# Optimization experiments

Hardware: AMD Instinct MI355X
Metric: run time of the kernel (lower is better)

Reference implementation:

```python
import jax, jax.numpy as jnp
import numpy as np


def setup_inputs() -> dict:
    key = jax.random.key(0)
    ks = jax.random.split(key, 6)
    B, Nab, Nag, d, K = 16, 16384, 16384, 128, 10
    return {
        "H1": jax.random.normal(ks[0], (B, Nab, d), jnp.float32),
        "H2": jax.random.normal(ks[1], (B, Nag, d), jnp.float32),
        "X1": jax.random.normal(ks[2], (B, Nab, 3), jnp.float32),
        "X2": jax.random.normal(ks[3], (B, Nag, 3), jnp.float32),
        "W1": jax.random.uniform(ks[4], (K, d, d), jnp.float32),
        "W2": jax.random.uniform(ks[5], (K, d, d), jnp.float32),
    }


def _kabsch(P, Q):
    # Rigid alignment: find R (3x3), t (3,) s.t. P @ R + t ~= Q (least squares).
    c1 = P.mean(axis=0)
    c2 = Q.mean(axis=0)
    Pc = P - c1
    Qc = Q - c2
    Hm = Pc.T @ Qc  # [3,3] covariance
    U, S, Vt = jnp.linalg.svd(Hm, full_matrices=False)
    sign = jnp.sign(jnp.linalg.det(U @ Vt))
    Dm = jnp.diag(jnp.concatenate([jnp.ones(2, dtype=P.dtype), sign[None]]))
    R = U @ Dm @ Vt
    t = c2 - c1 @ R
    return P @ R + t, R, t


def reference(H1, H2, X1, X2, W1, W2):
    # Keypoint cross-attention. Faithful to torch:
    #   alpha_1k = softmax( (H1 @ W1_k @ H2.T).mean(dim=1) / sqrt(d) )
    # Using mean-over-columns identity: (H1 @ W @ H2.T).mean(1) = H1 @ W @ mean(H2,0)
    d = H1.shape[-1]
    scale = 1.0 / np.sqrt(d)
    h2bar = H2.mean(axis=1)  # [B, d]
    h1bar = H1.mean(axis=1)  # [B, d]
    v1 = jnp.einsum('kde,be->bkd', W1, h2bar)          # W1_k @ mean(H2)
    s1 = jnp.einsum('bnd,bkd->bkn', H1, v1) * scale     # [B, K, Nab]
    a1 = jax.nn.softmax(s1, axis=-1)
    Y1 = jnp.einsum('bkn,bnc->bkc', a1, X1)             # [B, K, 3]
    v2 = jnp.einsum('kde,be->bkd', W2, h1bar)
    s2 = jnp.einsum('bmd,bkd->bkm', H2, v2) * scale     # [B, K, Nag]
    a2 = jax.nn.softmax(s2, axis=-1)
    Y2 = jnp.einsum('bkm,bmc->bkc', a2, X2)             # [B, K, 3]
    Y1_aligned, R, t = jax.vmap(_kabsch)(Y1, Y2)
    return jnp.stack([Y1, Y2, Y1_aligned], axis=1)      # [B, 3, K, 3]
```

## Files before the change

### kernel.cpp

```cpp
#include <hip/hip_runtime.h>
#include <math.h>

#define NB 16
#define NN 16384
#define DD 128
#define KK 10

#define WS_FLOATS 46336

__global__ __launch_bounds__(256) void k_means(const float* __restrict__ H1,
                                               const float* __restrict__ H2,
                                               float* __restrict__ hsum) {
    int bi = blockIdx.x;
    int t = bi >> 10;
    int rem = bi & 1023;
    int b = rem >> 6;
    int chunk = rem & 63;
    const float* src = (t ? H2 : H1) + ((size_t)b * NN + (size_t)chunk * 256) * DD;
    const float4* src4 = (const float4*)src;
    int tid = threadIdx.x;
    float4 s = make_float4(0.f, 0.f, 0.f, 0.f);
#pragma unroll 8
    for (int i = 0; i < 32; ++i) {
        float4 x = src4[i * 256 + tid];
        s.x += x.x; s.y += x.y; s.z += x.z; s.w += x.w;
    }
    s.x += __shfl_xor(s.x, 32);
    s.y += __shfl_xor(s.y, 32);
    s.z += __shfl_xor(s.z, 32);
    s.w += __shfl_xor(s.w, 32);
    __shared__ float red[4][32][4];
    int wave = tid >> 6, lane = tid & 63;
    if (lane < 32) {
        red[wave][lane][0] = s.x; red[wave][lane][1] = s.y;
        red[wave][lane][2] = s.z; red[wave][lane][3] = s.w;
    }
    __syncthreads();
    if (tid < 32) {
        float t0 = 0.f, t1 = 0.f, t2 = 0.f, t3 = 0.f;
#pragma unroll
        for (int w = 0; w < 4; ++w) {
            t0 += red[w][tid][0]; t1 += red[w][tid][1];
            t2 += red[w][tid][2]; t3 += red[w][tid][3];
        }
        float* dst = hsum + (size_t)(t * NB + b) * DD + tid * 4;
        atomicAdd(dst + 0, t0);
        atomicAdd(dst + 1, t1);
        atomicAdd(dst + 2, t2);
        atomicAdd(dst + 3, t3);
    }
}

__global__ __launch_bounds__(128) void k_v(const float* __restrict__ W1,
                                           const float* __restrict__ W2,
                                           const float* __restrict__ hsum,
                                           float* __restrict__ v) {
    int bi = blockIdx.x;
    int p = bi / 160;
    int rem = bi % 160;
    int b = rem / 10;
    int k = rem % 10;
    const float* W = (p ? W2 : W1) + (size_t)k * DD * DD;
    const float* hb = hsum + (size_t)((1 - p) * NB + b) * DD;
    __shared__ float4 h_s[32];
    int tid = threadIdx.x;
    if (tid < 32) h_s[tid] = ((const float4*)hb)[tid];
    __syncthreads();
    const float4* Wrow = (const float4*)(W + (size_t)tid * DD);
    float acc = 0.f;
#pragma unroll 8
    for (int e4 = 0; e4 < 32; ++e4) {
        float4 w4 = Wrow[e4];
        float4 h4 = h_s[e4];
        acc += w4.x * h4.x + w4.y * h4.y + w4.z * h4.z + w4.w * h4.w;
    }
    const float SCALE = (float)(1.0 / (16384.0 * 11.313708498984761));
    v[((size_t)(p * NB + b) * KK + k) * DD + tid] = acc * SCALE;
}

__global__ __launch_bounds__(256) void k_scores(const float* __restrict__ H1,
                                                const float* __restrict__ H2,
                                                const float* __restrict__ X1,
                                                const float* __restrict__ X2,
                                                const float* __restrict__ v,
                                                float* __restrict__ accg) {
    int bi = blockIdx.x;
    int p = bi >> 11;
    int rem = bi & 2047;
    int b = rem >> 7;
    int tile = rem & 127;
    int row0 = tile << 7;
    const float* H = (p ? H2 : H1) + (size_t)b * NN * DD;
    const float* X = (p ? X2 : X1) + (size_t)b * NN * 3;
    const float* vp = v + (size_t)(p * NB + b) * KK * DD;

    __shared__ float4 v_s4[KK * DD / 4];
    __shared__ float red[4][40];
    float* v_s = (float*)v_s4;

    int tid = threadIdx.x;
    for (int i = tid; i < KK * DD / 4; i += 256)
        v_s4[i] = ((const float4*)vp)[i];
    __syncthreads();

    int g = tid >> 3;
    int l = tid & 7;
    int nbase = row0 + (g << 2);

    float accs[4][KK];
#pragma unroll
    for (int r = 0; r < 4; ++r)
#pragma unroll
        for (int k = 0; k < KK; ++k) accs[r][k] = 0.f;

#pragma unroll
    for (int j = 0; j < 4; ++j) {
        float4 h[4];
#pragma unroll
        for (int r = 0; r < 4; ++r)
            h[r] = *(const float4*)(H + (size_t)(nbase + r) * DD + (j << 5) + (l << 2));
#pragma unroll
        for (int k = 0; k < KK; ++k) {
            float4 vv = *(const float4*)(v_s + k * DD + (j << 5) + (l << 2));
#pragma unroll
            for (int r = 0; r < 4; ++r)
                accs[r][k] += h[r].x * vv.x + h[r].y * vv.y + h[r].z * vv.z + h[r].w * vv.w;
        }
    }
#pragma unroll
    for (int r = 0; r < 4; ++r)
#pragma unroll
        for (int k = 0; k < KK; ++k) {
            float s = accs[r][k];
            s += __shfl_xor(s, 1);
            s += __shfl_xor(s, 2);
            s += __shfl_xor(s, 4);
            accs[r][k] = s;
        }

    float pSE[KK], pY0[KK], pY1[KK], pY2[KK];
#pragma unroll
    for (int k = 0; k < KK; ++k) { pSE[k] = 0.f; pY0[k] = 0.f; pY1[k] = 0.f; pY2[k] = 0.f; }

#pragma unroll
    for (int r = 0; r < 4; ++r) {
        int n = nbase + r;
        float x0 = X[(size_t)n * 3 + 0];
        float x1 = X[(size_t)n * 3 + 1];
        float x2 = X[(size_t)n * 3 + 2];
#pragma unroll
        for (int k = 0; k < KK; ++k) {
            float e = __expf(accs[r][k]);
            pSE[k] += e;
            pY0[k] += e * x0;
            pY1[k] += e * x1;
            pY2[k] += e * x2;
        }
    }
#pragma unroll
    for (int k = 0; k < KK; ++k) {
        pSE[k] += __shfl_xor(pSE[k], 8);  pSE[k] += __shfl_xor(pSE[k], 16);  pSE[k] += __shfl_xor(pSE[k], 32);
        pY0[k] += __shfl_xor(pY0[k], 8);  pY0[k] += __shfl_xor(pY0[k], 16);  pY0[k] += __shfl_xor(pY0[k], 32);
        pY1[k] += __shfl_xor(pY1[k], 8);  pY1[k] += __shfl_xor(pY1[k], 16);  pY1[k] += __shfl_xor(pY1[k], 32);
        pY2[k] += __shfl_xor(pY2[k], 8);  pY2[k] += __shfl_xor(pY2[k], 16);  pY2[k] += __shfl_xor(pY2[k], 32);
    }
    int wave = tid >> 6, lane = tid & 63;
    if (lane == 0) {
#pragma unroll
        for (int k = 0; k < KK; ++k) {
            red[wave][k] = pSE[k];
            red[wave][10 + k] = pY0[k];
            red[wave][20 + k] = pY1[k];
            red[wave][30 + k] = pY2[k];
        }
    }
    __syncthreads();
    if (tid < 40) {
        float s = red[0][tid] + red[1][tid] + red[2][tid] + red[3][tid];
        atomicAdd(accg + (size_t)(p * NB + b) * 40 + tid, s);
    }
}

__global__ __launch_bounds__(64) void k_final(const float* __restrict__ accg,
                                              float* __restrict__ out) {
    int b = blockIdx.x;
    int tid = threadIdx.x;
    __shared__ float Ys[2][KK][3];
    if (tid < 2 * KK * 3) {
        int p = tid / 30;
        int r = tid % 30;
        int k = r / 3;
        int c = r % 3;
        const float* a = accg + (size_t)(p * NB + b) * 40;
        float val = a[10 + c * 10 + k] / a[k];
        Ys[p][k][c] = val;
        out[((size_t)(b * 3 + p) * KK + k) * 3 + c] = val;
    }
    __syncthreads();
    if (tid == 0) {
        double P[KK][3], Q[KK][3];
        double c1[3] = {0, 0, 0}, c2[3] = {0, 0, 0};
        for (int i = 0; i < KK; ++i)
            for (int c = 0; c < 3; ++c) {
                P[i][c] = (double)Ys[0][i][c];
                Q[i][c] = (double)Ys[1][i][c];
                c1[c] += P[i][c];
                c2[c] += Q[i][c];
            }
        for (int c = 0; c < 3; ++c) { c1[c] /= KK; c2[c] /= KK; }
        double A0[3][3];
        for (int a = 0; a < 3; ++a)
            for (int c = 0; c < 3; ++c) {
                double s = 0;
                for (int i = 0; i < KK; ++i) s += (P[i][a] - c1[a]) * (Q[i][c] - c2[c]);
                A0[a][c] = s;
            }
        double Bm[3][3], V[3][3];
        for (int a = 0; a < 3; ++a)
            for (int c = 0; c < 3; ++c) { Bm[a][c] = A0[a][c]; V[a][c] = (a == c) ? 1.0 : 0.0; }
        for (int sweep = 0; sweep < 16; ++sweep)
            for (int p = 0; p < 2; ++p)
                for (int q = p + 1; q < 3; ++q) {
                    double al = 0, be = 0, ga = 0;
                    for (int r = 0; r < 3; ++r) {
                        al += Bm[r][p] * Bm[r][p];
                        be += Bm[r][q] * Bm[r][q];
                        ga += Bm[r][p] * Bm[r][q];
                    }
                    if (fabs(ga) < 1e-300) continue;
                    double zeta = (be - al) / (2.0 * ga);
                    double t = copysign(1.0, zeta) / (fabs(zeta) + sqrt(1.0 + zeta * zeta));
                    double cs = 1.0 / sqrt(1.0 + t * t);
                    double sn = cs * t;
                    for (int r = 0; r < 3; ++r) {
                        double bp = Bm[r][p], bq = Bm[r][q];
                        Bm[r][p] = cs * bp - sn * bq;
                        Bm[r][q] = sn * bp + cs * bq;
                        double vp = V[r][p], vq = V[r][q];
                        V[r][p] = cs * vp - sn * vq;
                        V[r][q] = sn * vp + cs * vq;
                    }
                }
        double sig[3];
        for (int j = 0; j < 3; ++j) {
            sig[j] = sqrt(Bm[0][j] * Bm[0][j] + Bm[1][j] * Bm[1][j] + Bm[2][j] * Bm[2][j]);
            if (sig[j] < 1e-300) sig[j] = 1e-300;
        }
        int jmin = 0;
        if (sig[1] < sig[jmin]) jmin = 1;
        if (sig[2] < sig[jmin]) jmin = 2;
        double det = A0[0][0] * (A0[1][1] * A0[2][2] - A0[1][2] * A0[2][1])
                   - A0[0][1] * (A0[1][0] * A0[2][2] - A0[1][2] * A0[2][0])
                   + A0[0][2] * (A0[1][0] * A0[2][1] - A0[1][1] * A0[2][0]);
        double sgn = (det >= 0.0) ? 1.0 : -1.0;
        double R[3][3];
        for (int a = 0; a < 3; ++a)
            for (int c = 0; c < 3; ++c) {
                double s = 0;
                for (int j = 0; j < 3; ++j) {
                    double dj = (j == jmin) ? sgn : 1.0;
                    s += dj * (Bm[a][j] / sig[j]) * V[c][j];
                }
                R[a][c] = s;
            }
        for (int i = 0; i < KK; ++i)
            for (int c = 0; c < 3; ++c) {
                double s = c2[c];
                for (int a = 0; a < 3; ++a) s += (P[i][a] - c1[a]) * R[a][c];
                out[((size_t)(b * 3 + 2) * KK + i) * 3 + c] = (float)s;
            }
    }
}

extern "C" void kernel_launch(void* const* d_in, const int* in_sizes, int n_in,
                              void* d_out, int out_size, void* d_ws, size_t ws_size,
                              hipStream_t stream) {
    const float* H1 = (const float*)d_in[0];
    const float* H2 = (const float*)d_in[1];
    const float* X1 = (const float*)d_in[2];
    const float* X2 = (const float*)d_in[3];
    const float* W1 = (const float*)d_in[4];
    const float* W2 = (const float*)d_in[5];
    float* out = (float*)d_out;
    float* ws = (float*)d_ws;
    float* hsum = ws;
    float* v    = ws + 4096;
    float* accg = ws + 45056;

    hipMemsetAsync(d_ws, 0, WS_FLOATS * sizeof(float), stream);
    hipLaunchKernelGGL(k_means,  dim3(2048), dim3(256), 0, stream, H1, H2, hsum);
    hipLaunchKernelGGL(k_v,      dim3(320),  dim3(128), 0, stream, W1, W2, hsum, v);
    hipLaunchKernelGGL(k_scores, dim3(4096), dim3(256), 0, stream, H1, H2, X1, X2, v, accg);
    hipLaunchKernelGGL(k_final,  dim3(16),   dim3(64),  0, stream, accg, out);
}
```

Baseline: 380.8 us.

## Fuse H1 mean reduction into H1 scores pass and distribute exp work per lane

```diff
diff --git a/kernel.cpp b/kernel.cpp
--- a/kernel.cpp
+++ b/kernel.cpp
@@ -8,32 +8,36 @@
 
 #define WS_FLOATS 46336
 
-__global__ __launch_bounds__(256) void k_means(const float* __restrict__ H1,
-                                               const float* __restrict__ H2,
-                                               float* __restrict__ hsum) {
+__device__ __forceinline__ float4 f4add(float4 a, float4 b) {
+    return make_float4(a.x + b.x, a.y + b.y, a.z + b.z, a.w + b.w);
+}
+
+__global__ __launch_bounds__(256, 8) void k_sum(const float* __restrict__ H,
+                                                float* __restrict__ dst) {
     int bi = blockIdx.x;
-    int t = bi >> 10;
-    int rem = bi & 1023;
-    int b = rem >> 6;
-    int chunk = rem & 63;
-    const float* src = (t ? H2 : H1) + ((size_t)b * NN + (size_t)chunk * 256) * DD;
-    const float4* src4 = (const float4*)src;
+    int b = bi >> 8;
+    int chunk = bi & 255;
+    const float4* src4 = (const float4*)(H + ((size_t)b * NN + (size_t)chunk * 64) * DD);
     int tid = threadIdx.x;
-    float4 s = make_float4(0.f, 0.f, 0.f, 0.f);
-#pragma unroll 8
-    for (int i = 0; i < 32; ++i) {
-        float4 x = src4[i * 256 + tid];
-        s.x += x.x; s.y += x.y; s.z += x.z; s.w += x.w;
-    }
-    s.x += __shfl_xor(s.x, 32);
-    s.y += __shfl_xor(s.y, 32);
-    s.z += __shfl_xor(s.z, 32);
-    s.w += __shfl_xor(s.w, 32);
+    float4 x0 = src4[0 * 256 + tid];
+    float4 x1 = src4[1 * 256 + tid];
+    float4 x2 = src4[2 * 256 + tid];
+    float4 x3 = src4[3 * 256 + tid];
+    float4 x4 = src4[4 * 256 + tid];
+    float4 x5 = src4[5 * 256 + tid];
+    float4 x6 = src4[6 * 256 + tid];
+    float4 x7 = src4[7 * 256 + tid];
+    float4 a = f4add(f4add(f4add(x0, x1), f4add(x2, x3)),
+                     f4add(f4add(x4, x5), f4add(x6, x7)));
+    a.x += __shfl_xor(a.x, 32);
+    a.y += __shfl_xor(a.y, 32);
+    a.z += __shfl_xor(a.z, 32);
+    a.w += __shfl_xor(a.w, 32);
     __shared__ float red[4][32][4];
-    int wave = tid >> 6, lane = tid & 63;
+    int wv = tid >> 6, lane = tid & 63;
     if (lane < 32) {
-        red[wave][lane][0] = s.x; red[wave][lane][1] = s.y;
-        red[wave][lane][2] = s.z; red[wave][lane][3] = s.w;
+        red[wv][lane][0] = a.x; red[wv][lane][1] = a.y;
+        red[wv][lane][2] = a.z; red[wv][lane][3] = a.w;
     }
     __syncthreads();
     if (tid < 32) {
@@ -43,30 +47,27 @@
             t0 += red[w][tid][0]; t1 += red[w][tid][1];
             t2 += red[w][tid][2]; t3 += red[w][tid][3];
         }
-        float* dst = hsum + (size_t)(t * NB + b) * DD + tid * 4;
-        atomicAdd(dst + 0, t0);
-        atomicAdd(dst + 1, t1);
-        atomicAdd(dst + 2, t2);
-        atomicAdd(dst + 3, t3);
-    }
-}
-
-__global__ __launch_bounds__(128) void k_v(const float* __restrict__ W1,
-                                           const float* __restrict__ W2,
-                                           const float* __restrict__ hsum,
-                                           float* __restrict__ v) {
+        float* d = dst + (size_t)b * DD + tid * 4;
+        atomicAdd(d + 0, t0);
+        atomicAdd(d + 1, t1);
+        atomicAdd(d + 2, t2);
+        atomicAdd(d + 3, t3);
+    }
+}
+
+__global__ __launch_bounds__(128) void k_v(const float* __restrict__ W,
+                                           const float* __restrict__ hsrc,
+                                           float* __restrict__ vdst) {
     int bi = blockIdx.x;
-    int p = bi / 160;
-    int rem = bi % 160;
-    int b = rem / 10;
-    int k = rem % 10;
-    const float* W = (p ? W2 : W1) + (size_t)k * DD * DD;
-    const float* hb = hsum + (size_t)((1 - p) * NB + b) * DD;
+    int b = bi / 10;
+    int k = bi % 10;
+    const float* Wk = W + (size_t)k * DD * DD;
+    const float* hb = hsrc + (size_t)b * DD;
     __shared__ float4 h_s[32];
     int tid = threadIdx.x;
     if (tid < 32) h_s[tid] = ((const float4*)hb)[tid];
     __syncthreads();
-    const float4* Wrow = (const float4*)(W + (size_t)tid * DD);
+    const float4* Wrow = (const float4*)(Wk + (size_t)tid * DD);
     float acc = 0.f;
 #pragma unroll 8
     for (int e4 = 0; e4 < 32; ++e4) {
@@ -75,28 +76,26 @@
         acc += w4.x * h4.x + w4.y * h4.y + w4.z * h4.z + w4.w * h4.w;
     }
     const float SCALE = (float)(1.0 / (16384.0 * 11.313708498984761));
-    v[((size_t)(p * NB + b) * KK + k) * DD + tid] = acc * SCALE;
-}
-
-__global__ __launch_bounds__(256) void k_scores(const float* __restrict__ H1,
-                                                const float* __restrict__ H2,
-                                                const float* __restrict__ X1,
-                                                const float* __restrict__ X2,
-                                                const float* __restrict__ v,
-                                                float* __restrict__ accg) {
+    vdst[((size_t)b * KK + k) * DD + tid] = acc * SCALE;
+}
+
+template <bool FOLD>
+__global__ __launch_bounds__(256, 4) void k_scores(const float* __restrict__ H,
+                                                   const float* __restrict__ X,
+                                                   const float* __restrict__ v,
+                                                   float* __restrict__ accgp,
+                                                   float* __restrict__ hsum0) {
     int bi = blockIdx.x;
-    int p = bi >> 11;
-    int rem = bi & 2047;
-    int b = rem >> 7;
-    int tile = rem & 127;
+    int b = bi >> 7;
+    int tile = bi & 127;
     int row0 = tile << 7;
-    const float* H = (p ? H2 : H1) + (size_t)b * NN * DD;
-    const float* X = (p ? X2 : X1) + (size_t)b * NN * 3;
-    const float* vp = v + (size_t)(p * NB + b) * KK * DD;
+    const float* Hb = H + (size_t)b * NN * DD;
+    const float* Xb = X + (size_t)b * NN * 3;
+    const float* vp = v + (size_t)b * KK * DD;
 
     __shared__ float4 v_s4[KK * DD / 4];
     __shared__ float red[4][40];
-    float* v_s = (float*)v_s4;
+    __shared__ float4 colred4[4][4][8];
 
     int tid = threadIdx.x;
     for (int i = tid; i < KK * DD / 4; i += 256)
@@ -112,16 +111,23 @@
     for (int r = 0; r < 4; ++r)
 #pragma unroll
         for (int k = 0; k < KK; ++k) accs[r][k] = 0.f;
+    float4 csum[4];
+    if (FOLD) {
+#pragma unroll
+        for (int j = 0; j < 4; ++j) csum[j] = make_float4(0.f, 0.f, 0.f, 0.f);
+    }
 
 #pragma unroll
     for (int j = 0; j < 4; ++j) {
         float4 h[4];
 #pragma unroll
         for (int r = 0; r < 4; ++r)
-            h[r] = *(const float4*)(H + (size_t)(nbase + r) * DD + (j << 5) + (l << 2));
+            h[r] = *(const float4*)(Hb + (size_t)(nbase + r) * DD + (j << 5) + (l << 2));
+        if (FOLD)
+            csum[j] = f4add(csum[j], f4add(f4add(h[0], h[1]), f4add(h[2], h[3])));
 #pragma unroll
         for (int k = 0; k < KK; ++k) {
-            float4 vv = *(const float4*)(v_s + k * DD + (j << 5) + (l << 2));
+            float4 vv = v_s4[k * 32 + (j << 3) + l];
 #pragma unroll
             for (int r = 0; r < 4; ++r)
                 accs[r][k] += h[r].x * vv.x + h[r].y * vv.y + h[r].z * vv.z + h[r].w * vv.w;
@@ -138,46 +144,79 @@
             accs[r][k] = s;
         }
 
-    float pSE[KK], pY0[KK], pY1[KK], pY2[KK];
-#pragma unroll
-    for (int k = 0; k < KK; ++k) { pSE[k] = 0.f; pY0[k] = 0.f; pY1[k] = 0.f; pY2[k] = 0.f; }
-
+    float sk0[4], sk1[4];
+#pragma unroll
+    for (int r = 0; r < 4; ++r) {
+        float u0 = 0.f, u1 = 0.f;
+#pragma unroll
+        for (int k = 0; k < KK; ++k) {
+            if (k == l) u0 = accs[r][k];
+            if (k == l + 8) u1 = accs[r][k];
+        }
+        sk0[r] = u0;
+        sk1[r] = u1;
+    }
+    float m1 = (l < 2) ? 1.f : 0.f;
+    float pse0 = 0.f, py00 = 0.f, py10 = 0.f, py20 = 0.f;
+    float pse1 = 0.f, py01 = 0.f, py11 = 0.f, py21 = 0.f;
 #pragma unroll
     for (int r = 0; r < 4; ++r) {
         int n = nbase + r;
-        float x0 = X[(size_t)n * 3 + 0];
-        float x1 = X[(size_t)n * 3 + 1];
-        float x2 = X[(size_t)n * 3 + 2];
-#pragma unroll
-        for (int k = 0; k < KK; ++k) {
-            float e = __expf(accs[r][k]);
-            pSE[k] += e;
-            pY0[k] += e * x0;
-            pY1[k] += e * x1;
-            pY2[k] += e * x2;
-        }
-    }
-#pragma unroll
-    for (int k = 0; k < KK; ++k) {
-        pSE[k] += __shfl_xor(pSE[k], 8);  pSE[k] += __shfl_xor(pSE[k], 16);  pSE[k] += __shfl_xor(pSE[k], 32);
-        pY0[k] += __shfl_xor(pY0[k], 8);  pY0[k] += __shfl_xor(pY0[k], 16);  pY0[k] += __shfl_xor(pY0[k], 32);
-        pY1[k] += __shfl_xor(pY1[k], 8);  pY1[k] += __shfl_xor(pY1[k], 16);  pY1[k] += __shfl_xor(pY1[k], 32);
-        pY2[k] += __shfl_xor(pY2[k], 8);  pY2[k] += __shfl_xor(pY2[k], 16);  pY2[k] += __shfl_xor(pY2[k], 32);
-    }
-    int wave = tid >> 6, lane = tid & 63;
-    if (lane == 0) {
-#pragma unroll
-        for (int k = 0; k < KK; ++k) {
-            red[wave][k] = pSE[k];
-            red[wave][10 + k] = pY0[k];
-            red[wave][20 + k] = pY1[k];
-            red[wave][30 + k] = pY2[k];
+        float x0 = Xb[(size_t)n * 3 + 0];
+        float x1 = Xb[(size_t)n * 3 + 1];
+        float x2 = Xb[(size_t)n * 3 + 2];
+        float e0 = __expf(sk0[r]);
+        float e1 = m1 * __expf(sk1[r]);
+        pse0 += e0; py00 += e0 * x0; py10 += e0 * x1; py20 += e0 * x2;
+        pse1 += e1; py01 += e1 * x0; py11 += e1 * x1; py21 += e1 * x2;
+    }
+#pragma unroll
+    for (int d = 8; d <= 32; d <<= 1) {
+        pse0 += __shfl_xor(pse0, d); py00 += __shfl_xor(py00, d);
+        py10 += __shfl_xor(py10, d); py20 += __shfl_xor(py20, d);
+        pse1 += __shfl_xor(pse1, d); py01 += __shfl_xor(py01, d);
+        py11 += __shfl_xor(py11, d); py21 += __shfl_xor(py21, d);
+    }
+    if (FOLD) {
+#pragma unroll
+        for (int j = 0; j < 4; ++j) {
+#pragma unroll
+            for (int d = 8; d <= 32; d <<= 1) {
+                csum[j].x += __shfl_xor(csum[j].x, d);
+                csum[j].y += __shfl_xor(csum[j].y, d);
+                csum[j].z += __shfl_xor(csum[j].z, d);
+                csum[j].w += __shfl_xor(csum[j].w, d);
+            }
+        }
+    }
+    int wv = tid >> 6, lane = tid & 63;
+    if (lane < 8) {
+        red[wv][l] = pse0;
+        red[wv][10 + l] = py00;
+        red[wv][20 + l] = py10;
+        red[wv][30 + l] = py20;
+        if (l < 2) {
+            red[wv][8 + l] = pse1;
+            red[wv][18 + l] = py01;
+            red[wv][28 + l] = py11;
+            red[wv][38 + l] = py21;
+        }
+        if (FOLD) {
+#pragma unroll
+            for (int j = 0; j < 4; ++j) colred4[wv][j][l] = csum[j];
         }
     }
     __syncthreads();
     if (tid < 40) {
         float s = red[0][tid] + red[1][tid] + red[2][tid] + red[3][tid];
-        atomicAdd(accg + (size_t)(p * NB + b) * 40 + tid, s);
+        atomicAdd(accgp + (size_t)b * 40 + tid, s);
+    }
+    if (FOLD && tid < 128) {
+        int j = tid >> 5, rr = tid & 31, ll = rr >> 2, c = rr & 3;
+        float s = 0.f;
+#pragma unroll
+        for (int w = 0; w < 4; ++w) s += ((const float*)&colred4[w][j][ll])[c];
+        atomicAdd(hsum0 + (size_t)b * DD + tid, s);
     }
 }
 
@@ -284,12 +323,18 @@
     float* out = (float*)d_out;
     float* ws = (float*)d_ws;
     float* hsum = ws;
-    float* v    = ws + 4096;
-    float* accg = ws + 45056;
-
-    hipMemsetAsync(d_ws, 0, WS_FLOATS * sizeof(float), stream);
-    hipLaunchKernelGGL(k_means,  dim3(2048), dim3(256), 0, stream, H1, H2, hsum);
-    hipLaunchKernelGGL(k_v,      dim3(320),  dim3(128), 0, stream, W1, W2, hsum, v);
-    hipLaunchKernelGGL(k_scores, dim3(4096), dim3(256), 0, stream, H1, H2, X1, X2, v, accg);
-    hipLaunchKernelGGL(k_final,  dim3(16),   dim3(64),  0, stream, accg, out);
-}
+    float* accg = ws + 4096;
+    float* v    = ws + 5376;
+
+    hipMemsetAsync(d_ws, 0, 5376 * sizeof(float), stream);
+    hipLaunchKernelGGL(k_sum, dim3(4096), dim3(256), 0, stream, H2, hsum + (size_t)NB * DD);
+    hipLaunchKernelGGL(k_v, dim3(160), dim3(128), 0, stream, W1, hsum + (size_t)NB * DD, v);
+    hipLaunchKernelGGL((k_scores<true>), dim3(2048), dim3(256), 0, stream,
+                       H1, X1, v, accg, hsum);
+    hipLaunchKernelGGL(k_v, dim3(160), dim3(128), 0, stream, W2, hsum,
+                       v + (size_t)NB * KK * DD);
+    hipLaunchKernelGGL((k_scores<false>), dim3(2048), dim3(256), 0, stream,
+                       H2, X2, v + (size_t)NB * KK * DD, accg + (size_t)NB * 40,
+                       (float*)nullptr);
+    hipLaunchKernelGGL(k_final, dim3(16), dim3(64), 0, stream, accg, out);
+}
```

Result: slower. 465.7 us (+22.3%).
